# Optimization experiments

Hardware: AMD Instinct MI355X
Metric: run time of the kernel (lower is better)

## Reference

```python
import jax, jax.numpy as jnp
import numpy as np
import math

BS, S, D = 1, 2048, 1024
H = 16
DK = D // H  # 64


def _log_sparse_neighbor_mask(seq_len):
    """mask[i,j]=True iff j==i, or j in [i-k, i) with k=seq_len//2, or i-j is a power of 2.
    Matches generate_log_sparse_plus_neighbors_mask(seq_len, seq_len//2)."""
    k = seq_len // 2
    i = jnp.arange(seq_len, dtype=jnp.int32)[:, None]
    j = jnp.arange(seq_len, dtype=jnp.int32)[None, :]
    diff = i - j
    neighbor = (diff >= 0) & (diff <= k)  # includes diagonal (diff==0)
    pow2 = (diff > 0) & ((diff & (diff - 1)) == 0)
    return neighbor | pow2  # [seq_len, seq_len] bool


def setup_inputs() -> dict:
    key = jax.random.key(0)
    ks = jax.random.split(key, 9)
    std = 0.02
    return {
        "Q": jax.random.normal(ks[0], (BS, S, D), dtype=jnp.float32),
        "Wq": jax.random.normal(ks[1], (D, H * DK), dtype=jnp.float32) * std,
        "bq": jnp.zeros((H * DK,), dtype=jnp.float32),
        "Wk": jax.random.normal(ks[2], (D, H * DK), dtype=jnp.float32) * std,
        "bk": jnp.zeros((H * DK,), dtype=jnp.float32),
        "Wv": jax.random.normal(ks[3], (D, H * DK), dtype=jnp.float32) * std,
        "bv": jnp.zeros((H * DK,), dtype=jnp.float32),
        "Wo": jax.random.normal(ks[4], (H * DK, D), dtype=jnp.float32) * std,
        "bo": jnp.zeros((D,), dtype=jnp.float32),
    }


def reference(Q, Wq, bq, Wk, bk, Wv, bv, Wo, bo):
    bs, s, d = Q.shape
    # QKV projections -> [bs, h, s, dk]
    q = (Q @ Wq + bq).reshape(bs, s, H, DK).transpose(0, 2, 1, 3)
    k = (Q @ Wk + bk).reshape(bs, s, H, DK).transpose(0, 2, 1, 3)
    v = (Q @ Wv + bv).reshape(bs, s, H, DK).transpose(0, 2, 1, 3)

    # log_sparse_attention: scale is 1/sqrt(d_k); mask regenerated internally
    mask = _log_sparse_neighbor_mask(s)  # [s, s] bool
    scores = jnp.einsum("bhqd,bhkd->bhqk", q, k) / math.sqrt(DK)
    scores = jnp.where(mask[None, None, :, :], scores, -jnp.inf)
    attn = jax.nn.softmax(scores, axis=-1)  # [bs, h, s, s]
    out = jnp.einsum("bhqk,bhkd->bhqd", attn, v)

    # merge heads + output projection
    out = out.transpose(0, 2, 1, 3).reshape(bs, s, H * DK)
    out = out @ Wo + bo
    return (out, attn)
```

## Files before the change

### kernel.cpp

```cpp
#include <hip/hip_runtime.h>

#define SEQ 2048
#define DM 1024
#define NH 16
#define DKH 64
#define BAND 1024
#define QKV 3072
#define PBW 1064

typedef __attribute__((ext_vector_type(8))) __bf16 bf16x8;
typedef __attribute__((ext_vector_type(4))) __bf16 bf16x4;
typedef __attribute__((ext_vector_type(4))) float f32x4;

static __device__ __forceinline__ f32x4 mfma16(bf16x8 a, bf16x8 b, f32x4 c) {
  return __builtin_amdgcn_mfma_f32_16x16x32_bf16(a, b, c, 0, 0, 0);
}

#define GLOAD16(gp, lp)                                                        \
  __builtin_amdgcn_global_load_lds(                                            \
      (const __attribute__((address_space(1))) void*)(gp),                     \
      (__attribute__((address_space(3))) void*)(lp), 16, 0, 0)

struct PrepArgs {
  const float* win[4];
  __bf16* wout[4];
  const float* Q;
  __bf16* Qb;
};
__global__ void prep(PrepArgs P) {
  int z = blockIdx.z;
  if (z < 4) {
    __shared__ float t[32][33];
    const float* in = P.win[z];
    __bf16* out = P.wout[z];
    int c0 = blockIdx.x * 32, r0 = blockIdx.y * 32;
    int tx = threadIdx.x, ty = threadIdx.y;
    for (int r = ty; r < 32; r += 8)
      t[r][tx] = in[(size_t)(r0 + r) * DM + c0 + tx];
    __syncthreads();
    for (int r = ty; r < 32; r += 8)
      out[(size_t)(c0 + r) * DM + r0 + tx] = (__bf16)t[tx][r];
  } else {
    int t = threadIdx.y * 32 + threadIdx.x;
    int base = (blockIdx.y * 32 + blockIdx.x) * 512 + t;
#pragma unroll
    for (int u = 0; u < 2; u++) {
      int i = base + u * 256;
      float4 v = reinterpret_cast<const float4*>(P.Q)[i];
      bf16x4 o = {(__bf16)v.x, (__bf16)v.y, (__bf16)v.z, (__bf16)v.w};
      reinterpret_cast<bf16x4*>(P.Qb)[i] = o;
    }
  }
}

template <int BM, int BN, bool BF16OUT, bool VOUT>
__global__ __launch_bounds__(256) void gemm_lds(
    const __bf16* __restrict__ A, const __bf16* __restrict__ BT,
    const float* __restrict__ b0, const float* __restrict__ b1,
    const float* __restrict__ b2, float* __restrict__ Cf,
    __bf16* __restrict__ Cb, __bf16* __restrict__ VT, int M, int N, int K) {
  constexpr int BK = 32;
  constexpr int FM = BM / 32;
  constexpr int FN = BN / 32;
  __shared__ __bf16 lA[2][BM * BK];
  __shared__ __bf16 lB[2][BN * BK];
  int tid = threadIdx.x;
  int lane = tid & 63;
  int l15 = lane & 15, lg = lane >> 4;
  int w = tid >> 6;
  int nwg = gridDim.x * gridDim.y;
  int bid = blockIdx.y * gridDim.x + blockIdx.x;
  int swz = (bid & 7) * (nwg >> 3) + (bid >> 3);
  int bx = swz % gridDim.x;
  int by = swz / gridDim.x;
  int row0 = by * BM;
  int col0 = bx * BN;
  int sec = col0 >> 10;
  const float* bias = sec == 0 ? b0 : (sec == 1 ? b1 : b2);
  int cbase = col0 & (DM - 1);
  int wr = (w >> 1) * (BM / 2);
  int wc = (w & 1) * (BN / 2);
  f32x4 acc[FM][FN] = {};
  const __bf16* aSrc = A + ((size_t)row0 + (tid >> 2)) * K + (tid & 3) * 8;
  const __bf16* bSrc = BT + ((size_t)col0 + (tid >> 2)) * K + (tid & 3) * 8;

  auto stage = [&](int b, int kk) {
#pragma unroll
    for (int s = 0; s < BM / 64; s++)
      GLOAD16(aSrc + (size_t)s * 64 * K + kk, (char*)lA[b] + tid * 16 + s * 4096);
#pragma unroll
    for (int s = 0; s < BN / 64; s++)
      GLOAD16(bSrc + (size_t)s * 64 * K + kk, (char*)lB[b] + tid * 16 + s * 4096);
  };

  stage(0, 0);
  __syncthreads();
  int cur = 0;
  for (int kk = 0; kk < K; kk += BK) {
    if (kk + BK < K) stage(cur ^ 1, kk + BK);
    bf16x8 af[FM], bfr[FN];
#pragma unroll
    for (int mi = 0; mi < FM; mi++)
      af[mi] = *(const bf16x8*)&lA[cur][(wr + mi * 16 + l15) * BK + lg * 8];
#pragma unroll
    for (int ni = 0; ni < FN; ni++)
      bfr[ni] = *(const bf16x8*)&lB[cur][(wc + ni * 16 + l15) * BK + lg * 8];
#pragma unroll
    for (int mi = 0; mi < FM; mi++)
#pragma unroll
      for (int ni = 0; ni < FN; ni++)
        acc[mi][ni] = mfma16(af[mi], bfr[ni], acc[mi][ni]);
    __syncthreads();
    cur ^= 1;
  }
  if (VOUT && sec == 2) {
#pragma unroll
    for (int mi = 0; mi < FM; mi++) {
      int row = row0 + wr + mi * 16 + lg * 4;
#pragma unroll
      for (int ni = 0; ni < FN; ni++) {
        int hd = cbase + wc + ni * 16 + l15;
        float b = bias[hd];
        bf16x4 pk;
#pragma unroll
        for (int r = 0; r < 4; r++) pk[r] = (__bf16)(acc[mi][ni][r] + b);
        *(bf16x4*)&VT[(size_t)hd * SEQ + row] = pk;
      }
    }
    return;
  }
#pragma unroll
  for (int mi = 0; mi < FM; mi++) {
    int row = row0 + wr + mi * 16 + lg * 4;
#pragma unroll
    for (int ni = 0; ni < FN; ni++) {
      int col = col0 + wc + ni * 16 + l15;
      float b = bias[(cbase + wc + ni * 16 + l15) & (DM - 1)];
#pragma unroll
      for (int r = 0; r < 4; r++) {
        float v = acc[mi][ni][r] + b;
        if constexpr (BF16OUT)
          Cb[(size_t)(row + r) * N + col] = (__bf16)v;
        else
          Cf[(size_t)(row + r) * N + col] = v;
      }
    }
  }
}

__global__ __launch_bounds__(256) void attn_fused(
    const __bf16* __restrict__ qkvb, const __bf16* __restrict__ VT,
    float* __restrict__ attn_out, __bf16* __restrict__ pvb) {
  __shared__ __bf16 pbuf[16][PBW];
  __shared__ float wsum[4][16];
  __shared__ float sinv[16];

  int nwg = gridDim.x * gridDim.y;
  int bid = blockIdx.y * gridDim.x + blockIdx.x;
  int swz = (bid & 7) * (nwg >> 3) + (bid >> 3);
  int h = swz / (SEQ / 16);
  int i0 = (swz % (SEQ / 16)) * 16;

  int tid = threadIdx.x, lane = tid & 63, w = tid >> 6;
  int l15 = lane & 15, lg = lane >> 4;

  int jlo = i0 - BAND;
  if (jlo < 0) jlo = 0;
  int ntiles = (i0 + 16 - jlo) >> 4;
  int ktiles = (ntiles + 1) & ~1;
  int n = ntiles * 16;

  const __bf16* qptr = qkvb + (size_t)(i0 + l15) * QKV + h * DKH + lg * 8;
  bf16x8 aq0 = *(const bf16x8*)qptr;
  bf16x8 aq1 = *(const bf16x8*)(qptr + 32);
  const __bf16* kbase = qkvb + DM + h * DKH + lg * 8;

  float sm[4] = {0.f, 0.f, 0.f, 0.f};
  for (int t = w; t < ntiles; t += 4) {
    int jb = jlo + t * 16;
    const __bf16* kptr = kbase + (size_t)(jb + l15) * QKV;
    f32x4 acc = {0.f, 0.f, 0.f, 0.f};
    acc = mfma16(aq0, *(const bf16x8*)kptr, acc);
    acc = mfma16(aq1, *(const bf16x8*)(kptr + 32), acc);
    int col = jb + l15;
    int x = jb - jlo + l15;
#pragma unroll
    for (int r = 0; r < 4; r++) {
      int i = i0 + lg * 4 + r;
      float e = 0.f;
      if (col <= i && i - col <= BAND) {
        e = __expf(acc[r] * 0.125f);
        sm[r] += e;
      }
      pbuf[lg * 4 + r][x] = (__bf16)e;
    }
  }
  if (ktiles != ntiles) pbuf[tid >> 4][n + (tid & 15)] = (__bf16)0.f;
#pragma unroll
  for (int o = 1; o < 16; o <<= 1)
#pragma unroll
    for (int r = 0; r < 4; r++) sm[r] += __shfl_xor(sm[r], o);
  if (l15 == 0)
#pragma unroll
    for (int r = 0; r < 4; r++) wsum[w][lg * 4 + r] = sm[r];
  __syncthreads();
  if (tid < 16)
    sinv[tid] = 1.f / (wsum[0][tid] + wsum[1][tid] + wsum[2][tid] + wsum[3][tid]);
  __syncthreads();

  f32x4* abase = (f32x4*)(attn_out + ((size_t)h * SEQ + i0) * SEQ);
  for (int idx = tid; idx < 16 * (SEQ / 4); idx += 256) {
    int row = idx >> 9;
    int j4 = idx & 511;
    int x = j4 * 4 - jlo;
    bool valid = (unsigned)x < (unsigned)n;
    int xc = valid ? x : 0;
    bf16x4 v4 = *(const bf16x4*)&pbuf[row][xc];
    float inv = valid ? sinv[row] : 0.f;
    f32x4 o = {(float)v4[0] * inv, (float)v4[1] * inv, (float)v4[2] * inv,
               (float)v4[3] * inv};
    __builtin_nontemporal_store(o, abase + idx);
  }

  f32x4 acc = {0.f, 0.f, 0.f, 0.f};
  int d0 = w * 16;
  const __bf16* vtp = VT + ((size_t)h * DKH + d0 + l15) * SEQ;
  for (int kt = 0; kt < ktiles; kt += 2) {
    int kk = kt * 16;
    bf16x8 pa = *(const bf16x8*)&pbuf[l15][kk + lg * 8];
    int jj = jlo + kk + lg * 8;
    bf16x8 vf = {};
    if (jj < SEQ) vf = *(const bf16x8*)(vtp + jj);
    acc = mfma16(pa, vf, acc);
  }
#pragma unroll
  for (int r = 0; r < 4; r++) {
    int row = lg * 4 + r;
    float inv = sinv[row];
    pvb[(size_t)(i0 + row) * DM + h * DKH + d0 + l15] = (__bf16)(acc[r] * inv);
  }
}

extern "C" void kernel_launch(void* const* d_in, const int* in_sizes, int n_in,
                              void* d_out, int out_size, void* d_ws,
                              size_t ws_size, hipStream_t stream) {
  const float* Q = (const float*)d_in[0];
  const float* Wq = (const float*)d_in[1];
  const float* bq = (const float*)d_in[2];
  const float* Wk = (const float*)d_in[3];
  const float* bk = (const float*)d_in[4];
  const float* Wv = (const float*)d_in[5];
  const float* bv = (const float*)d_in[6];
  const float* Wo = (const float*)d_in[7];
  const float* bo = (const float*)d_in[8];
  float* out_proj = (float*)d_out;
  float* attn_out = out_proj + (size_t)SEQ * DM;

  char* ws = (char*)d_ws;
  size_t off = 0;
  auto alloc = [&](size_t bytes) {
    void* p = ws + off;
    off = (off + bytes + 255) & ~(size_t)255;
    return p;
  };
  __bf16* Qb    = (__bf16*)alloc((size_t)SEQ * DM * 2);
  __bf16* WqkvT = (__bf16*)alloc((size_t)QKV * DM * 2);
  __bf16* WoT   = (__bf16*)alloc((size_t)DM * DM * 2);
  __bf16* qkvb  = (__bf16*)alloc((size_t)SEQ * QKV * 2);
  __bf16* VT    = (__bf16*)alloc((size_t)NH * DKH * SEQ * 2);
  __bf16* pvb   = (__bf16*)alloc((size_t)SEQ * DM * 2);

  PrepArgs P;
  P.win[0] = Wq; P.win[1] = Wk; P.win[2] = Wv; P.win[3] = Wo;
  P.wout[0] = WqkvT;
  P.wout[1] = WqkvT + (size_t)DM * DM;
  P.wout[2] = WqkvT + (size_t)2 * DM * DM;
  P.wout[3] = WoT;
  P.Q = Q;
  P.Qb = Qb;
  prep<<<dim3(32, 32, 5), dim3(32, 8), 0, stream>>>(P);

  gemm_lds<64, 128, true, true><<<dim3(QKV / 128, SEQ / 64), 256, 0, stream>>>(
      Qb, WqkvT, bq, bk, bv, nullptr, qkvb, VT, SEQ, QKV, DM);

  attn_fused<<<dim3(SEQ / 16, NH), 256, 0, stream>>>(qkvb, VT, attn_out, pvb);

  gemm_lds<64, 64, false, false><<<dim3(DM / 64, SEQ / 64), 256, 0, stream>>>(
      pvb, WoT, bo, bo, bo, out_proj, nullptr, nullptr, SEQ, DM, DM);
}
```

Baseline: 127.1 us.

## Double K tile to 64 with XOR-swizzled LDS and prefetch-two pipeline

The projection GEMM now uses a K tile of 64, which halves the number of loop iterations and barriers. It stores tiles in LDS with an XOR swizzle on 16-byte chunks to avoid bank conflicts when fragments are read. Loads are issued two stages ahead, with explicit vmcnt waits and raw s_barrier in place of __syncthreads. LDS use doubles, which may lower occupancy, and the hand-written waitcnt logic depends on the exact number of loads issued per stage.

```diff
diff --git a/kernel.cpp b/kernel.cpp
--- a/kernel.cpp
+++ b/kernel.cpp
@@ -59,9 +59,11 @@
     const float* __restrict__ b0, const float* __restrict__ b1,
     const float* __restrict__ b2, float* __restrict__ Cf,
     __bf16* __restrict__ Cb, __bf16* __restrict__ VT, int M, int N, int K) {
-  constexpr int BK = 32;
+  constexpr int BK = 64;
   constexpr int FM = BM / 32;
   constexpr int FN = BN / 32;
+  constexpr int LA = BM * BK * 2 / (256 * 16);
+  constexpr int LB = BN * BK * 2 / (256 * 16);
   __shared__ __bf16 lA[2][BM * BK];
   __shared__ __bf16 lB[2][BN * BK];
   int tid = threadIdx.x;
@@ -81,38 +83,63 @@
   int wr = (w >> 1) * (BM / 2);
   int wc = (w & 1) * (BN / 2);
   f32x4 acc[FM][FN] = {};
-  const __bf16* aSrc = A + ((size_t)row0 + (tid >> 2)) * K + (tid & 3) * 8;
-  const __bf16* bSrc = BT + ((size_t)col0 + (tid >> 2)) * K + (tid & 3) * 8;
-
-  auto stage = [&](int b, int kk) {
-#pragma unroll
-    for (int s = 0; s < BM / 64; s++)
-      GLOAD16(aSrc + (size_t)s * 64 * K + kk, (char*)lA[b] + tid * 16 + s * 4096);
-#pragma unroll
-    for (int s = 0; s < BN / 64; s++)
-      GLOAD16(bSrc + (size_t)s * 64 * K + kk, (char*)lB[b] + tid * 16 + s * 4096);
+
+  auto stage = [&](int b, int kt) {
+#pragma unroll
+    for (int s = 0; s < LA; s++) {
+      int u = tid + s * 256;
+      int r = u >> 3;
+      int cc = (u & 7) ^ (r & 7);
+      GLOAD16(A + (size_t)(row0 + r) * K + kt * BK + cc * 8,
+              (char*)lA[b] + u * 16);
+    }
+#pragma unroll
+    for (int s = 0; s < LB; s++) {
+      int u = tid + s * 256;
+      int r = u >> 3;
+      int cc = (u & 7) ^ (r & 7);
+      GLOAD16(BT + (size_t)(col0 + r) * K + kt * BK + cc * 8,
+              (char*)lB[b] + u * 16);
+    }
   };
 
+  const int T = K / BK;
   stage(0, 0);
-  __syncthreads();
-  int cur = 0;
-  for (int kk = 0; kk < K; kk += BK) {
-    if (kk + BK < K) stage(cur ^ 1, kk + BK);
-    bf16x8 af[FM], bfr[FN];
-#pragma unroll
-    for (int mi = 0; mi < FM; mi++)
-      af[mi] = *(const bf16x8*)&lA[cur][(wr + mi * 16 + l15) * BK + lg * 8];
-#pragma unroll
-    for (int ni = 0; ni < FN; ni++)
-      bfr[ni] = *(const bf16x8*)&lB[cur][(wc + ni * 16 + l15) * BK + lg * 8];
-#pragma unroll
-    for (int mi = 0; mi < FM; mi++)
-#pragma unroll
-      for (int ni = 0; ni < FN; ni++)
-        acc[mi][ni] = mfma16(af[mi], bfr[ni], acc[mi][ni]);
-    __syncthreads();
-    cur ^= 1;
-  }
+  stage(1, 1);
+  for (int t = 0; t < T; t++) {
+    if (t + 1 < T)
+      asm volatile("s_waitcnt vmcnt(%0)" ::"i"(LA + LB) : "memory");
+    else
+      asm volatile("s_waitcnt vmcnt(0)" ::: "memory");
+    __builtin_amdgcn_s_barrier();
+    int cur = t & 1;
+    bf16x8 af[2][FM], bfr[2][FN];
+#pragma unroll
+    for (int kh = 0; kh < 2; kh++) {
+#pragma unroll
+      for (int mi = 0; mi < FM; mi++) {
+        int r = wr + mi * 16 + l15;
+        af[kh][mi] = *(const bf16x8*)((const char*)lA[cur] + r * 128 +
+                                      ((((kh << 2) | lg) ^ (r & 7)) << 4));
+      }
+#pragma unroll
+      for (int ni = 0; ni < FN; ni++) {
+        int r = wc + ni * 16 + l15;
+        bfr[kh][ni] = *(const bf16x8*)((const char*)lB[cur] + r * 128 +
+                                       ((((kh << 2) | lg) ^ (r & 7)) << 4));
+      }
+    }
+#pragma unroll
+    for (int kh = 0; kh < 2; kh++)
+#pragma unroll
+      for (int mi = 0; mi < FM; mi++)
+#pragma unroll
+        for (int ni = 0; ni < FN; ni++)
+          acc[mi][ni] = mfma16(af[kh][mi], bfr[kh][ni], acc[mi][ni]);
+    __builtin_amdgcn_s_barrier();
+    if (t + 2 < T) stage(cur, t + 2);
+  }
+
   if (VOUT && sec == 2) {
 #pragma unroll
     for (int mi = 0; mi < FM; mi++) {
```

Result: faster. 120.5 us (-5.2%).
